# Kernel optimization log

Hardware: AMD Instinct MI355X
Metric: run time of the kernel (lower is better)

Reference implementation:

```python
import jax, jax.numpy as jnp
import numpy as np

N = 131072      # total nodes in batch
D = 128         # input_dim
K_EXP = 1024    # input_dim * num_conv_kernels
H = 512         # cluster_model_hidden_dim
NG = 4          # number of groups (sub-models)
F_SEG = 8192    # fine clusters (global_max_pool segments)
G_SEG = 32      # coarse graphs (InstanceNorm segments)
C = 16          # node_num_classes
EPS = 1e-5      # InstanceNorm eps


def setup_inputs() -> dict:
    key = jax.random.key(0)
    ks = jax.random.split(key, 8)
    x = jax.random.normal(ks[0], (N, D), jnp.float32)
    # disjoint partition of node indices into NG groups (gather/scatter dispatch)
    group_indices = jax.random.permutation(ks[1], N).reshape(NG, N // NG)
    # sorted segment ids, every segment non-empty
    pool_cluster_fine = (jnp.arange(N) // (N // F_SEG)).astype(jnp.int32)
    batch_cluster_coarse = (jnp.arange(F_SEG) // (F_SEG // G_SEG)).astype(jnp.int32)
    # per-group NodeModel params: expand D -> K_EXP, relu, project -> H
    W1 = jax.random.normal(ks[2], (NG, D, K_EXP), jnp.float32) * (1.0 / np.sqrt(D))
    b1 = jnp.zeros((NG, K_EXP), jnp.float32)
    W2 = jax.random.normal(ks[3], (NG, K_EXP, H), jnp.float32) * (1.0 / np.sqrt(K_EXP))
    b2 = jnp.zeros((NG, H), jnp.float32)
    # classifier (glorot weight, zero bias)
    w_out = jax.random.normal(ks[4], (H, C), jnp.float32) * np.sqrt(2.0 / (H + C))
    b_out = jnp.zeros((C,), jnp.float32)
    return {"x": x, "group_indices": group_indices,
            "pool_cluster_fine": pool_cluster_fine,
            "batch_cluster_coarse": batch_cluster_coarse,
            "W1": W1, "b1": b1, "W2": W2, "b2": b2,
            "w_out": w_out, "b_out": b_out}


def reference(x, group_indices, pool_cluster_fine, batch_cluster_coarse,
              W1, b1, W2, b2, w_out, b_out):
    # per-group gather -> sub-model -> scatter (vectorized over groups)
    xg = x[group_indices]                                   # [NG, N/NG, D]
    h = jax.nn.relu(jnp.einsum('gnd,gdk->gnk', xg, W1) + b1[:, None, :])
    og = jnp.einsum('gnk,gkh->gnh', h, W2) + b2[:, None, :]  # [NG, N/NG, H]
    new_feat = jnp.zeros((x.shape[0], H), x.dtype).at[group_indices.reshape(-1)].set(
        og.reshape(-1, H))                                   # [N, H]
    # global_max_pool over fine clusters
    emb = jax.ops.segment_max(new_feat, pool_cluster_fine,
                              num_segments=F_SEG, indices_are_sorted=True)  # [F, H]
    # PyG InstanceNorm(affine=False): per coarse-graph, per-channel standardization
    ones = jnp.ones((F_SEG, 1), emb.dtype)
    cnt = jax.ops.segment_sum(ones, batch_cluster_coarse,
                              num_segments=G_SEG, indices_are_sorted=True)  # [G,1]
    mean = jax.ops.segment_sum(emb, batch_cluster_coarse,
                               num_segments=G_SEG, indices_are_sorted=True) / cnt
    var = jax.ops.segment_sum(emb * emb, batch_cluster_coarse,
                              num_segments=G_SEG, indices_are_sorted=True) / cnt - mean ** 2
    normed = (emb - mean[batch_cluster_coarse]) * jax.lax.rsqrt(var[batch_cluster_coarse] + EPS)
    # dropout is identity in eval mode; classifier
    logits = normed @ w_out + b_out                          # [F, C]
    return logits
```

## Files before the change

### kernel.cpp

```cpp
#include <hip/hip_runtime.h>
#include <stdint.h>

typedef __bf16 bf16;
typedef bf16 bf16x4 __attribute__((ext_vector_type(4)));
typedef bf16 bf16x8 __attribute__((ext_vector_type(8)));
typedef float f32x4 __attribute__((ext_vector_type(4)));

#define N_NODES 131072
#define D_IN    128
#define KEXP    1024
#define H_DIM   512
#define NGRP    4
#define NPG     32768
#define F_SEG   8192
#define G_SEG   32
#define C_OUT   16

typedef const __attribute__((address_space(1))) void* gas_t;
typedef __attribute__((address_space(3))) void* las_t;
__device__ __forceinline__ void cp16_async(const bf16* g, bf16* l) {
    __builtin_amdgcn_global_load_lds((gas_t)g, (las_t)l, 16, 0, 0);
}

__global__ void convert_weights(const float* __restrict__ W1,
                                const float* __restrict__ W2,
                                bf16* __restrict__ W1F,
                                bf16* __restrict__ W2F)
{
    int t = blockIdx.x * 256 + threadIdx.x;
    if (t < 65536) {
        int slot = t & 63, f = (t >> 6) & 7, kc = (t >> 9) & 31, g = t >> 14;
        int ks = f >> 1, kt = f & 1, quad = slot >> 4, ln = slot & 15;
        int k = kc * 32 + kt * 16 + ln;
        const float* src = W1 + ((size_t)(g * 128 + ks * 32 + quad * 8)) * 1024 + k;
        bf16x8 v;
        #pragma unroll
        for (int j = 0; j < 8; ++j) v[j] = (bf16)src[(size_t)j * 1024];
        *(bf16x8*)(W1F + (size_t)t * 8) = v;
    } else {
        int u = t - 65536;
        if (u < 262144) {
            int slot = u & 63, f = (u >> 6) & 15, kc = (u >> 10) & 31;
            int n0t2 = (u >> 15) & 1, g = u >> 16;
            int quad = slot >> 4, ln = slot & 15;
            int k = kc * 32 + quad * 8;
            int n = n0t2 * 256 + f * 16 + ln;
            const float* src = W2 + ((size_t)(g * 1024 + k)) * 512 + n;
            bf16x8 v;
            #pragma unroll
            for (int j = 0; j < 8; ++j) v[j] = (bf16)src[(size_t)j * 512];
            *(bf16x8*)(W2F + (size_t)u * 8) = v;
        }
    }
}

__global__ __launch_bounds__(256, 2)
void mlp_kernel(const float* __restrict__ x,
                const int*   __restrict__ gidx,
                const bf16*  __restrict__ W1F,
                const float* __restrict__ b1,
                const bf16*  __restrict__ W2F,
                const float* __restrict__ b2,
                bf16*        __restrict__ NF)
{
    __shared__ __align__(16) bf16 sW1[2][4096];
    __shared__ __align__(16) bf16 sH[2][4096];
    __shared__ __align__(16) float sB1[1024];

    const int tid  = threadIdx.x;
    const int bid  = blockIdx.x;
    const int g    = bid >> 9;
    const int rem  = bid & 511;
    const int m0   = (rem >> 1) * 128;
    const int n0t2 = rem & 1;

    const int wave = tid >> 6;
    const int lane = tid & 63;
    const int quad = lane >> 4;
    const int ln   = lane & 15;
    const int mg   = wave >> 1;
    const int ng   = wave & 1;

    const int*  gI  = gidx + g * NPG + m0;
    const bf16* W1g = W1F + (size_t)g * 131072;
    const bf16* W2g = W2F + (size_t)(g * 2 + n0t2) * 262144;

    bf16x8 xf[8];
    #pragma unroll
    for (int i = 0; i < 8; ++i) {
        int row  = wave * 32 + (i >> 2) * 16 + ln;
        int node = gI[row];
        const float* src = x + (size_t)node * D_IN + (i & 3) * 32 + quad * 8;
        float4 a = *(const float4*)src;
        float4 b = *(const float4*)(src + 4);
        bf16x8 v;
        v[0] = (bf16)a.x; v[1] = (bf16)a.y; v[2] = (bf16)a.z; v[3] = (bf16)a.w;
        v[4] = (bf16)b.x; v[5] = (bf16)b.y; v[6] = (bf16)b.z; v[7] = (bf16)b.w;
        xf[i] = v;
    }

    *(float4*)(sB1 + tid * 4) = *(const float4*)(b1 + g * KEXP + tid * 4);

    f32x4 acc2[4][8];
    #pragma unroll
    for (int a = 0; a < 4; ++a)
        #pragma unroll
        for (int b = 0; b < 8; ++b)
            acc2[a][b] = (f32x4){0.f, 0.f, 0.f, 0.f};

    auto do_stage1 = [&](int j) {
        const bf16* w1buf = sW1[j & 1];
        bf16*       hdst  = sH[j & 1];
        f32x4 acc1[2][2];
        #pragma unroll
        for (int a = 0; a < 2; ++a)
            #pragma unroll
            for (int b = 0; b < 2; ++b)
                acc1[a][b] = (f32x4){0.f, 0.f, 0.f, 0.f};
        #pragma unroll
        for (int ks = 0; ks < 4; ++ks) {
            #pragma unroll
            for (int kt = 0; kt < 2; ++kt) {
                bf16x8 w1f = *(const bf16x8*)(w1buf + ((ks * 2 + kt) * 64 + lane) * 8);
                #pragma unroll
                for (int mt = 0; mt < 2; ++mt)
                    acc1[kt][mt] = __builtin_amdgcn_mfma_f32_16x16x32_bf16(
                        w1f, xf[mt * 4 + ks], acc1[kt][mt], 0, 0, 0);
            }
        }
        #pragma unroll
        for (int kt = 0; kt < 2; ++kt) {
            float4 bv = *(const float4*)(sB1 + j * 32 + kt * 16 + quad * 4);
            float bvr[4] = {bv.x, bv.y, bv.z, bv.w};
            int qa = kt * 2 + (quad >> 1);
            int j0 = (quad & 1) * 4;
            #pragma unroll
            for (int mt = 0; mt < 2; ++mt) {
                int fm = wave * 2 + mt;
                bf16x4 pk;
                #pragma unroll
                for (int reg = 0; reg < 4; ++reg)
                    pk[reg] = (bf16)fmaxf(acc1[kt][mt][reg] + bvr[reg], 0.f);
                *(bf16x4*)(hdst + (fm * 64 + qa * 16 + ln) * 8 + j0) = pk;
            }
        }
    };

    __syncthreads();

    #pragma unroll
    for (int r = 0; r < 2; ++r) {
        int c = r * 4 + wave;
        cp16_async(W1g + c * 512 + lane * 8, sW1[0] + c * 512);
    }
    #pragma unroll
    for (int r = 0; r < 2; ++r) {
        int c = r * 4 + wave;
        cp16_async(W1g + 4096 + c * 512 + lane * 8, sW1[1] + c * 512);
    }
    asm volatile("s_waitcnt vmcnt(2)" ::: "memory");
    __builtin_amdgcn_s_barrier();

    do_stage1(0);

    #pragma unroll 1
    for (int j = 1; j < 32; ++j) {
        __syncthreads();

        bf16x8 bb[8];
        {
            const bf16* w2src = W2g + (size_t)(j - 1) * 8192 + ng * 4096;
            #pragma unroll
            for (int nt = 0; nt < 8; ++nt)
                bb[nt] = *(const bf16x8*)(w2src + nt * 512 + lane * 8);
        }

        {
            int nkc = (j + 1) & 31;
            const bf16* w1src = W1g + (size_t)nkc * 4096;
            bf16* d1 = sW1[(j + 1) & 1];
            #pragma unroll
            for (int r = 0; r < 2; ++r) {
                int c = r * 4 + wave;
                cp16_async(w1src + c * 512 + lane * 8, d1 + c * 512);
            }
        }

        __builtin_amdgcn_s_setprio(1);
        do_stage1(j);

        {
            const bf16* hbuf = sH[(j - 1) & 1];
            #pragma unroll
            for (int mt = 0; mt < 4; ++mt) {
                bf16x8 a2 = *(const bf16x8*)(hbuf + ((mg * 4 + mt) * 64 + lane) * 8);
                #pragma unroll
                for (int nt = 0; nt < 8; ++nt)
                    acc2[mt][nt] = __builtin_amdgcn_mfma_f32_16x16x32_bf16(
                        a2, bb[nt], acc2[mt][nt], 0, 0, 0);
            }
        }
        __builtin_amdgcn_s_setprio(0);
    }

    __syncthreads();
    {
        bf16x8 bb[8];
        const bf16* w2src = W2g + (size_t)31 * 8192 + ng * 4096;
        #pragma unroll
        for (int nt = 0; nt < 8; ++nt)
            bb[nt] = *(const bf16x8*)(w2src + nt * 512 + lane * 8);
        const bf16* hbuf = sH[1];
        #pragma unroll
        for (int mt = 0; mt < 4; ++mt) {
            bf16x8 a2 = *(const bf16x8*)(hbuf + ((mg * 4 + mt) * 64 + lane) * 8);
            #pragma unroll
            for (int nt = 0; nt < 8; ++nt)
                acc2[mt][nt] = __builtin_amdgcn_mfma_f32_16x16x32_bf16(
                    a2, bb[nt], acc2[mt][nt], 0, 0, 0);
        }
    }

    const float* b2g = b2 + g * H_DIM + n0t2 * 256 + ng * 128;
    float b2v[8];
    #pragma unroll
    for (int nt = 0; nt < 8; ++nt) b2v[nt] = b2g[nt * 16 + ln];

    #pragma unroll
    for (int mt = 0; mt < 4; ++mt)
        #pragma unroll
        for (int reg = 0; reg < 4; ++reg) {
            int row  = mg * 64 + mt * 16 + quad * 4 + reg;
            int node = gI[row];
            bf16* dst = NF + (size_t)node * H_DIM + n0t2 * 256 + ng * 128;
            #pragma unroll
            for (int nt = 0; nt < 8; ++nt)
                dst[nt * 16 + ln] = (bf16)(acc2[mt][nt][reg] + b2v[nt]);
        }
}

__global__ void pool_kernel(const bf16* __restrict__ NF, float* __restrict__ EMB)
{
    int t  = blockIdx.x * 256 + threadIdx.x;
    int f  = t >> 6;
    int c8 = (t & 63) * 8;
    const uint4* src = (const uint4*)(NF + (size_t)f * 16 * 512 + c8);
    float m[8];
    #pragma unroll
    for (int i = 0; i < 8; ++i) m[i] = -INFINITY;
    #pragma unroll
    for (int r = 0; r < 16; ++r) {
        uint4 v = src[(size_t)r * 64];
        uint32_t w[4] = {v.x, v.y, v.z, v.w};
        #pragma unroll
        for (int i = 0; i < 4; ++i) {
            m[2*i]   = fmaxf(m[2*i],   __uint_as_float(w[i] << 16));
            m[2*i+1] = fmaxf(m[2*i+1], __uint_as_float(w[i] & 0xffff0000u));
        }
    }
    float* dst = EMB + (size_t)f * 512 + c8;
    *(float4*)dst       = make_float4(m[0], m[1], m[2], m[3]);
    *(float4*)(dst + 4) = make_float4(m[4], m[5], m[6], m[7]);
}

__global__ void stats_kernel(const float* __restrict__ EMB,
                             float* __restrict__ MEAN,
                             float* __restrict__ RSIG)
{
    int gc = blockIdx.x;
    int ch = blockIdx.y * 128 + threadIdx.x;
    const float* p = EMB + (size_t)gc * 256 * 512 + ch;
    float s = 0.f, ss = 0.f;
    #pragma unroll 4
    for (int r = 0; r < 256; ++r) {
        float v = p[(size_t)r * 512];
        s += v; ss += v * v;
    }
    float mean = s * (1.f / 256.f);
    float var  = ss * (1.f / 256.f) - mean * mean;
    MEAN[gc * 512 + ch] = mean;
    RSIG[gc * 512 + ch] = rsqrtf(var + 1e-5f);
}

__global__ __launch_bounds__(256)
void classifier_kernel(const float* __restrict__ EMB,
                       const float* __restrict__ MEAN,
                       const float* __restrict__ RSIG,
                       const float* __restrict__ w_out,
                       const float* __restrict__ b_out,
                       float* __restrict__ out)
{
    __shared__ float sW[512 * 16];
    __shared__ float sE[16 * 513];
    int t  = threadIdx.x;
    int f0 = blockIdx.x * 16;
    int gc = f0 >> 8;

    #pragma unroll
    for (int it = 0; it < 8; ++it) {
        int i = (it * 256 + t) * 4;
        *(float4*)(sW + i) = *(const float4*)(w_out + i);
    }
    #pragma unroll
    for (int it = 0; it < 32; ++it) {
        int i  = it * 256 + t;
        int fr = i >> 9;
        int h  = i & 511;
        float v = EMB[(size_t)(f0 + fr) * 512 + h];
        sE[fr * 513 + h] = (v - MEAN[gc * 512 + h]) * RSIG[gc * 512 + h];
    }
    __syncthreads();

    int fr = t >> 4;
    int c  = t & 15;
    float acc = b_out[c];
    #pragma unroll 8
    for (int h = 0; h < 512; ++h)
        acc += sE[fr * 513 + h] * sW[h * 16 + c];
    out[(size_t)(f0 + fr) * 16 + c] = acc;
}

extern "C" void kernel_launch(void* const* d_in, const int* in_sizes, int n_in,
                              void* d_out, int out_size, void* d_ws, size_t ws_size,
                              hipStream_t stream)
{
    const float* x     = (const float*)d_in[0];
    const int*   gidx  = (const int*)d_in[1];
    const float* W1    = (const float*)d_in[4];
    const float* b1    = (const float*)d_in[5];
    const float* W2    = (const float*)d_in[6];
    const float* b2    = (const float*)d_in[7];
    const float* w_out = (const float*)d_in[8];
    const float* b_out = (const float*)d_in[9];
    float* out = (float*)d_out;

    char* w = (char*)d_ws;
    bf16* W1F = (bf16*)w;  w += (size_t)NGRP * KEXP * D_IN * 2;
    bf16* W2F = (bf16*)w;  w += (size_t)NGRP * H_DIM * KEXP * 2;
    bf16* NF  = (bf16*)w;  w += (size_t)N_NODES * H_DIM * 2;
    float* EMB  = (float*)w; w += (size_t)F_SEG * H_DIM * 4;
    float* MEAN = (float*)w; w += (size_t)G_SEG * H_DIM * 4;
    float* RSIG = (float*)w; w += (size_t)G_SEG * H_DIM * 4;

    convert_weights<<<1280, 256, 0, stream>>>(W1, W2, W1F, W2F);
    mlp_kernel<<<2048, 256, 0, stream>>>(x, gidx, W1F, b1, W2F, b2, NF);
    pool_kernel<<<2048, 256, 0, stream>>>(NF, EMB);
    stats_kernel<<<dim3(32, 4), 128, 0, stream>>>(EMB, MEAN, RSIG);
    classifier_kernel<<<512, 256, 0, stream>>>(EMB, MEAN, RSIG, w_out, b_out, out);
}
```

Before: 358.2 us.

## Widen MLP block to full H with 8 waves and phased stage-2 scheduling

Each block now covers all 512 output columns for 128 rows using 512 threads (8 waves), instead of two blocks each computing half of H. This removes the duplicated stage-1 (x·W1) computation and x gather that the old split into column halves required. The K loop now takes 64-wide chunks (16 iterations), with explicit barriers, sched_barriers and setprio phases that interleave W2 loads and LDS reads with MFMA groups. In exchange it doubles LDS usage, adds many block-wide barriers, and raises register pressure per wave.

```diff
diff --git a/kernel.cpp b/kernel.cpp
--- a/kernel.cpp
+++ b/kernel.cpp
@@ -54,7 +54,7 @@
     }
 }
 
-__global__ __launch_bounds__(256, 2)
+__global__ __launch_bounds__(512, 2)
 void mlp_kernel(const float* __restrict__ x,
                 const int*   __restrict__ gidx,
                 const bf16*  __restrict__ W1F,
@@ -63,43 +63,49 @@
                 const float* __restrict__ b2,
                 bf16*        __restrict__ NF)
 {
-    __shared__ __align__(16) bf16 sW1[2][4096];
-    __shared__ __align__(16) bf16 sH[2][4096];
+    __shared__ __align__(16) bf16 sW1[2][8192];
+    __shared__ __align__(16) bf16 sH[2][8192];
     __shared__ __align__(16) float sB1[1024];
 
     const int tid  = threadIdx.x;
     const int bid  = blockIdx.x;
-    const int g    = bid >> 9;
-    const int rem  = bid & 511;
-    const int m0   = (rem >> 1) * 128;
-    const int n0t2 = rem & 1;
+    const int g    = bid >> 8;
+    const int m0   = (bid & 255) * 128;
 
     const int wave = tid >> 6;
     const int lane = tid & 63;
     const int quad = lane >> 4;
     const int ln   = lane & 15;
-    const int mg   = wave >> 1;
-    const int ng   = wave & 1;
+
+    const int rfA  = wave & 3;
+    const int rfB  = rfA + 4;
+    const int ktp  = (wave >> 2) * 2;
+    const int fbase = (wave >> 2) * 8;
+    const int mg   = wave & 1;
+    const int ng   = wave >> 1;
 
     const int*  gI  = gidx + g * NPG + m0;
     const bf16* W1g = W1F + (size_t)g * 131072;
-    const bf16* W2g = W2F + (size_t)(g * 2 + n0t2) * 262144;
-
-    bf16x8 xf[8];
-    #pragma unroll
-    for (int i = 0; i < 8; ++i) {
-        int row  = wave * 32 + (i >> 2) * 16 + ln;
-        int node = gI[row];
-        const float* src = x + (size_t)node * D_IN + (i & 3) * 32 + quad * 8;
-        float4 a = *(const float4*)src;
-        float4 b = *(const float4*)(src + 4);
-        bf16x8 v;
-        v[0] = (bf16)a.x; v[1] = (bf16)a.y; v[2] = (bf16)a.z; v[3] = (bf16)a.w;
-        v[4] = (bf16)b.x; v[5] = (bf16)b.y; v[6] = (bf16)b.z; v[7] = (bf16)b.w;
-        xf[i] = v;
-    }
-
-    *(float4*)(sB1 + tid * 4) = *(const float4*)(b1 + g * KEXP + tid * 4);
+    const bf16* W2g2 = W2F + ((size_t)(g * 2 + (ng >> 1))) * 262144 + (ng & 1) * 4096;
+
+    bf16x8 xf[2][4];
+    #pragma unroll
+    for (int r = 0; r < 2; ++r) {
+        int rf   = r ? rfB : rfA;
+        int node = gI[rf * 16 + ln];
+        #pragma unroll
+        for (int ks = 0; ks < 4; ++ks) {
+            const float* src = x + (size_t)node * D_IN + ks * 32 + quad * 8;
+            float4 a = *(const float4*)src;
+            float4 b = *(const float4*)(src + 4);
+            bf16x8 v;
+            v[0] = (bf16)a.x; v[1] = (bf16)a.y; v[2] = (bf16)a.z; v[3] = (bf16)a.w;
+            v[4] = (bf16)b.x; v[5] = (bf16)b.y; v[6] = (bf16)b.z; v[7] = (bf16)b.w;
+            xf[r][ks] = v;
+        }
+    }
+
+    *(float2*)(sB1 + tid * 2) = *(const float2*)(b1 + g * KEXP + tid * 2);
 
     f32x4 acc2[4][8];
     #pragma unroll
@@ -108,120 +114,193 @@
         for (int b = 0; b < 8; ++b)
             acc2[a][b] = (f32x4){0.f, 0.f, 0.f, 0.f};
 
-    auto do_stage1 = [&](int j) {
-        const bf16* w1buf = sW1[j & 1];
-        bf16*       hdst  = sH[j & 1];
-        f32x4 acc1[2][2];
-        #pragma unroll
-        for (int a = 0; a < 2; ++a)
-            #pragma unroll
-            for (int b = 0; b < 2; ++b)
-                acc1[a][b] = (f32x4){0.f, 0.f, 0.f, 0.f};
-        #pragma unroll
-        for (int ks = 0; ks < 4; ++ks) {
+    auto do_pack = [&](int j, bf16* hdst, const f32x4 (&acc1)[2][2]) {
+        #pragma unroll
+        for (int r = 0; r < 2; ++r) {
+            int rf = r ? rfB : rfA;
             #pragma unroll
             for (int kt = 0; kt < 2; ++kt) {
-                bf16x8 w1f = *(const bf16x8*)(w1buf + ((ks * 2 + kt) * 64 + lane) * 8);
-                #pragma unroll
-                for (int mt = 0; mt < 2; ++mt)
-                    acc1[kt][mt] = __builtin_amdgcn_mfma_f32_16x16x32_bf16(
-                        w1f, xf[mt * 4 + ks], acc1[kt][mt], 0, 0, 0);
-            }
-        }
-        #pragma unroll
-        for (int kt = 0; kt < 2; ++kt) {
-            float4 bv = *(const float4*)(sB1 + j * 32 + kt * 16 + quad * 4);
-            float bvr[4] = {bv.x, bv.y, bv.z, bv.w};
-            int qa = kt * 2 + (quad >> 1);
-            int j0 = (quad & 1) * 4;
-            #pragma unroll
-            for (int mt = 0; mt < 2; ++mt) {
-                int fm = wave * 2 + mt;
+                int kt2 = ktp + kt;
+                float4 bv = *(const float4*)(sB1 + j * 64 + kt2 * 16 + quad * 4);
+                float bvr[4] = {bv.x, bv.y, bv.z, bv.w};
+                int ks2 = kt2 >> 1;
+                int qa  = (kt2 & 1) * 2 + (quad >> 1);
+                int j0  = (quad & 1) * 4;
                 bf16x4 pk;
                 #pragma unroll
                 for (int reg = 0; reg < 4; ++reg)
-                    pk[reg] = (bf16)fmaxf(acc1[kt][mt][reg] + bvr[reg], 0.f);
-                *(bf16x4*)(hdst + (fm * 64 + qa * 16 + ln) * 8 + j0) = pk;
+                    pk[reg] = (bf16)fmaxf(acc1[r][kt][reg] + bvr[reg], 0.f);
+                *(bf16x4*)(hdst + ((rf * 2 + ks2) * 64 + qa * 16 + ln) * 8 + j0) = pk;
             }
         }
     };
 
+    auto s2row = [&](f32x4 (&acc)[8], bf16x8 a2v, const bf16x8 (&bb)[8]) {
+        #pragma unroll
+        for (int nt = 0; nt < 8; ++nt)
+            acc[nt] = __builtin_amdgcn_mfma_f32_16x16x32_bf16(a2v, bb[nt], acc[nt], 0, 0, 0);
+    };
+
     __syncthreads();
 
     #pragma unroll
     for (int r = 0; r < 2; ++r) {
-        int c = r * 4 + wave;
+        int c = r * 8 + wave;
         cp16_async(W1g + c * 512 + lane * 8, sW1[0] + c * 512);
     }
     #pragma unroll
     for (int r = 0; r < 2; ++r) {
-        int c = r * 4 + wave;
-        cp16_async(W1g + 4096 + c * 512 + lane * 8, sW1[1] + c * 512);
+        int c = r * 8 + wave;
+        cp16_async(W1g + 8192 + c * 512 + lane * 8, sW1[1] + c * 512);
     }
     asm volatile("s_waitcnt vmcnt(2)" ::: "memory");
     __builtin_amdgcn_s_barrier();
 
-    do_stage1(0);
+    {
+        bf16x8 w1f[8];
+        #pragma unroll
+        for (int f = 0; f < 8; ++f)
+            w1f[f] = *(const bf16x8*)(sW1[0] + ((fbase + f) * 64 + lane) * 8);
+        asm volatile("s_waitcnt lgkmcnt(0)" ::: "memory");
+        __builtin_amdgcn_sched_barrier(0);
+        f32x4 acc1[2][2];
+        #pragma unroll
+        for (int a = 0; a < 2; ++a)
+            #pragma unroll
+            for (int b = 0; b < 2; ++b)
+                acc1[a][b] = (f32x4){0.f, 0.f, 0.f, 0.f};
+        #pragma unroll
+        for (int ks = 0; ks < 4; ++ks)
+            #pragma unroll
+            for (int kt = 0; kt < 2; ++kt)
+                #pragma unroll
+                for (int r = 0; r < 2; ++r)
+                    acc1[r][kt] = __builtin_amdgcn_mfma_f32_16x16x32_bf16(
+                        w1f[ks * 2 + kt], xf[r][ks], acc1[r][kt], 0, 0, 0);
+        do_pack(0, sH[0], acc1);
+    }
+    asm volatile("s_waitcnt vmcnt(0)" ::: "memory");
+    __builtin_amdgcn_s_barrier();
 
     #pragma unroll 1
-    for (int j = 1; j < 32; ++j) {
-        __syncthreads();
-
-        bf16x8 bb[8];
+    for (int j = 1; j < 16; ++j) {
+        const int jm = j - 1;
+        const bf16* w1buf = sW1[j & 1];
+        bf16*       sHw   = sH[j & 1];
+        const bf16* sHr   = sH[jm & 1];
+        const bf16* w2a   = W2g2 + (size_t)(2 * jm) * 8192;
+        const bf16* w2b   = w2a + 8192;
+
+        bf16x8 bba[8];
+        #pragma unroll
+        for (int nt = 0; nt < 8; ++nt)
+            bba[nt] = *(const bf16x8*)(w2a + nt * 512 + lane * 8);
         {
-            const bf16* w2src = W2g + (size_t)(j - 1) * 8192 + ng * 4096;
-            #pragma unroll
-            for (int nt = 0; nt < 8; ++nt)
-                bb[nt] = *(const bf16x8*)(w2src + nt * 512 + lane * 8);
-        }
-
-        {
-            int nkc = (j + 1) & 31;
-            const bf16* w1src = W1g + (size_t)nkc * 4096;
-            bf16* d1 = sW1[(j + 1) & 1];
+            int nj = (j + 1) & 15;
+            const bf16* src = W1g + (size_t)nj * 8192;
+            bf16* dst = sW1[(j + 1) & 1];
             #pragma unroll
             for (int r = 0; r < 2; ++r) {
-                int c = r * 4 + wave;
-                cp16_async(w1src + c * 512 + lane * 8, d1 + c * 512);
+                int c = r * 8 + wave;
+                cp16_async(src + c * 512 + lane * 8, dst + c * 512);
             }
         }
-
+        bf16x8 w1f[8];
+        #pragma unroll
+        for (int f = 0; f < 8; ++f)
+            w1f[f] = *(const bf16x8*)(w1buf + ((fbase + f) * 64 + lane) * 8);
+        __builtin_amdgcn_s_barrier();
+        asm volatile("s_waitcnt lgkmcnt(0)" ::: "memory");
+        __builtin_amdgcn_sched_barrier(0);
         __builtin_amdgcn_s_setprio(1);
-        do_stage1(j);
-
-        {
-            const bf16* hbuf = sH[(j - 1) & 1];
-            #pragma unroll
-            for (int mt = 0; mt < 4; ++mt) {
-                bf16x8 a2 = *(const bf16x8*)(hbuf + ((mg * 4 + mt) * 64 + lane) * 8);
+        f32x4 acc1[2][2];
+        #pragma unroll
+        for (int a = 0; a < 2; ++a)
+            #pragma unroll
+            for (int b = 0; b < 2; ++b)
+                acc1[a][b] = (f32x4){0.f, 0.f, 0.f, 0.f};
+        #pragma unroll
+        for (int ks = 0; ks < 4; ++ks)
+            #pragma unroll
+            for (int kt = 0; kt < 2; ++kt)
                 #pragma unroll
-                for (int nt = 0; nt < 8; ++nt)
-                    acc2[mt][nt] = __builtin_amdgcn_mfma_f32_16x16x32_bf16(
-                        a2, bb[nt], acc2[mt][nt], 0, 0, 0);
-            }
-        }
+                for (int r = 0; r < 2; ++r)
+                    acc1[r][kt] = __builtin_amdgcn_mfma_f32_16x16x32_bf16(
+                        w1f[ks * 2 + kt], xf[r][ks], acc1[r][kt], 0, 0, 0);
         __builtin_amdgcn_s_setprio(0);
-    }
-
-    __syncthreads();
+        __builtin_amdgcn_s_barrier();
+
+        do_pack(j, sHw, acc1);
+        bf16x8 a00 = *(const bf16x8*)(sHr + (((mg * 4 + 0) * 2 + 0) * 64 + lane) * 8);
+        bf16x8 a01 = *(const bf16x8*)(sHr + (((mg * 4 + 1) * 2 + 0) * 64 + lane) * 8);
+        __builtin_amdgcn_s_barrier();
+        asm volatile("s_waitcnt lgkmcnt(0)" ::: "memory");
+        __builtin_amdgcn_sched_barrier(0);
+        __builtin_amdgcn_s_setprio(1);
+        s2row(acc2[0], a00, bba);
+        s2row(acc2[1], a01, bba);
+        __builtin_amdgcn_s_setprio(0);
+        __builtin_amdgcn_s_barrier();
+
+        bf16x8 bbb[8];
+        #pragma unroll
+        for (int nt = 0; nt < 8; ++nt)
+            bbb[nt] = *(const bf16x8*)(w2b + nt * 512 + lane * 8);
+        bf16x8 a02 = *(const bf16x8*)(sHr + (((mg * 4 + 2) * 2 + 0) * 64 + lane) * 8);
+        bf16x8 a03 = *(const bf16x8*)(sHr + (((mg * 4 + 3) * 2 + 0) * 64 + lane) * 8);
+        __builtin_amdgcn_s_barrier();
+        asm volatile("s_waitcnt lgkmcnt(0)" ::: "memory");
+        __builtin_amdgcn_sched_barrier(0);
+        __builtin_amdgcn_s_setprio(1);
+        s2row(acc2[2], a02, bba);
+        s2row(acc2[3], a03, bba);
+        __builtin_amdgcn_s_setprio(0);
+        __builtin_amdgcn_s_barrier();
+
+        bf16x8 a10 = *(const bf16x8*)(sHr + (((mg * 4 + 0) * 2 + 1) * 64 + lane) * 8);
+        bf16x8 a11 = *(const bf16x8*)(sHr + (((mg * 4 + 1) * 2 + 1) * 64 + lane) * 8);
+        __builtin_amdgcn_s_barrier();
+        asm volatile("s_waitcnt lgkmcnt(0)" ::: "memory");
+        __builtin_amdgcn_sched_barrier(0);
+        __builtin_amdgcn_s_setprio(1);
+        s2row(acc2[0], a10, bbb);
+        s2row(acc2[1], a11, bbb);
+        __builtin_amdgcn_s_setprio(0);
+        __builtin_amdgcn_s_barrier();
+
+        bf16x8 a12 = *(const bf16x8*)(sHr + (((mg * 4 + 2) * 2 + 1) * 64 + lane) * 8);
+        bf16x8 a13 = *(const bf16x8*)(sHr + (((mg * 4 + 3) * 2 + 1) * 64 + lane) * 8);
+        asm volatile("s_waitcnt vmcnt(0)" ::: "memory");
+        __builtin_amdgcn_s_barrier();
+        asm volatile("s_waitcnt lgkmcnt(0)" ::: "memory");
+        __builtin_amdgcn_sched_barrier(0);
+        __builtin_amdgcn_s_setprio(1);
+        s2row(acc2[2], a12, bbb);
+        s2row(acc2[3], a13, bbb);
+        __builtin_amdgcn_s_setprio(0);
+        __builtin_amdgcn_s_barrier();
+    }
+
     {
-        bf16x8 bb[8];
-        const bf16* w2src = W2g + (size_t)31 * 8192 + ng * 4096;
-        #pragma unroll
-        for (int nt = 0; nt < 8; ++nt)
-            bb[nt] = *(const bf16x8*)(w2src + nt * 512 + lane * 8);
-        const bf16* hbuf = sH[1];
+        const bf16* sHr = sH[1];
+        const bf16* w2a = W2g2 + (size_t)30 * 8192;
+        const bf16* w2b = w2a + 8192;
+        bf16x8 bba[8], bbb[8];
+        #pragma unroll
+        for (int nt = 0; nt < 8; ++nt) {
+            bba[nt] = *(const bf16x8*)(w2a + nt * 512 + lane * 8);
+            bbb[nt] = *(const bf16x8*)(w2b + nt * 512 + lane * 8);
+        }
         #pragma unroll
         for (int mt = 0; mt < 4; ++mt) {
-            bf16x8 a2 = *(const bf16x8*)(hbuf + ((mg * 4 + mt) * 64 + lane) * 8);
-            #pragma unroll
-            for (int nt = 0; nt < 8; ++nt)
-                acc2[mt][nt] = __builtin_amdgcn_mfma_f32_16x16x32_bf16(
-                    a2, bb[nt], acc2[mt][nt], 0, 0, 0);
-        }
-    }
-
-    const float* b2g = b2 + g * H_DIM + n0t2 * 256 + ng * 128;
+            bf16x8 a20 = *(const bf16x8*)(sHr + (((mg * 4 + mt) * 2 + 0) * 64 + lane) * 8);
+            bf16x8 a21 = *(const bf16x8*)(sHr + (((mg * 4 + mt) * 2 + 1) * 64 + lane) * 8);
+            s2row(acc2[mt], a20, bba);
+            s2row(acc2[mt], a21, bbb);
+        }
+    }
+
+    const float* b2g = b2 + g * H_DIM + ng * 128;
     float b2v[8];
     #pragma unroll
     for (int nt = 0; nt < 8; ++nt) b2v[nt] = b2g[nt * 16 + ln];
@@ -232,7 +311,7 @@
         for (int reg = 0; reg < 4; ++reg) {
             int row  = mg * 64 + mt * 16 + quad * 4 + reg;
             int node = gI[row];
-            bf16* dst = NF + (size_t)node * H_DIM + n0t2 * 256 + ng * 128;
+            bf16* dst = NF + (size_t)node * H_DIM + ng * 128;
             #pragma unroll
             for (int nt = 0; nt < 8; ++nt)
                 dst[nt * 16 + ln] = (bf16)(acc2[mt][nt][reg] + b2v[nt]);
@@ -343,7 +422,7 @@
     float* RSIG = (float*)w; w += (size_t)G_SEG * H_DIM * 4;
 
     convert_weights<<<1280, 256, 0, stream>>>(W1, W2, W1F, W2F);
-    mlp_kernel<<<2048, 256, 0, stream>>>(x, gidx, W1F, b1, W2F, b2, NF);
+    mlp_kernel<<<1024, 512, 0, stream>>>(x, gidx, W1F, b1, W2F, b2, NF);
     pool_kernel<<<2048, 256, 0, stream>>>(NF, EMB);
     stats_kernel<<<dim3(32, 4), 128, 0, stream>>>(EMB, MEAN, RSIG);
     classifier_kernel<<<512, 256, 0, stream>>>(EMB, MEAN, RSIG, w_out, b_out, out);
```

After: 379.3 us. +5.9%, slower.
